# Kernel tuning notes

Hardware: AMD Instinct MI355X
Metric: run time of the kernel (lower is better)

The kernel has to match this reference:

```python
import jax, jax.numpy as jnp
import numpy as np

N_NODES = 100000


def gcn_conv(x, src, dst, W, b):
    # PyG GCNConv: add self-loops, symmetric deg^-1/2 normalization,
    # linear transform, scatter-add aggregation to target nodes, plus bias.
    n = x.shape[0]
    loops = jnp.arange(n, dtype=src.dtype)
    s = jnp.concatenate([src, loops])
    d = jnp.concatenate([dst, loops])
    deg = jax.ops.segment_sum(jnp.ones_like(s, dtype=x.dtype), d, num_segments=n)
    dinv = jnp.where(deg > 0, jax.lax.rsqrt(deg), 0.0)
    norm = dinv[s] * dinv[d]                       # [E+n]
    h = x @ W                                      # [n, out]
    msg = h[s] * norm[:, None]                     # gather + scale
    out = jax.ops.segment_sum(msg, d, num_segments=n)
    return out + b


def setup_inputs() -> dict:
    key = jax.random.key(0)
    k1, k2, k3, k4 = jax.random.split(key, 4)
    in_c, hid_c, out_c = 64, 64, 64
    n_edges = 1600000
    x = jax.random.normal(k1, (N_NODES, in_c), dtype=jnp.float32)
    edge_index = jax.random.randint(k2, (2, n_edges), 0, N_NODES, dtype=jnp.int64)
    W1 = jax.random.normal(k3, (in_c, hid_c), dtype=jnp.float32) * (1.0 / np.sqrt(in_c))
    b1 = jnp.zeros((hid_c,), dtype=jnp.float32)
    W2 = jax.random.normal(k4, (hid_c, out_c), dtype=jnp.float32) * (1.0 / np.sqrt(hid_c))
    b2 = jnp.zeros((out_c,), dtype=jnp.float32)
    return {"x": x, "edge_index": edge_index, "W1": W1, "b1": b1, "W2": W2, "b2": b2}


def reference(x, edge_index, W1, b1, W2, b2):
    src, dst = edge_index[0], edge_index[1]
    h = gcn_conv(x, src, dst, W1, b1)
    h = jax.nn.relu(h)
    out = gcn_conv(h, src, dst, W2, b2)
    return out
```

## Files before the change

### kernel.cpp

```cpp
#include <hip/hip_runtime.h>

#define NCH 64
#define NBLK 512
#define CB 512

typedef unsigned int uint;
typedef short short8 __attribute__((ext_vector_type(8)));
typedef float floatx4 __attribute__((ext_vector_type(4)));

__device__ inline uint bf16rne(float f) {
    uint u = __float_as_uint(f);
    return (u + 0x7fffu + ((u >> 16) & 1u)) >> 16;
}
__device__ inline uint pack2bf(float lo, float hi) {
    return bf16rne(lo) | (bf16rne(hi) << 16);
}
__device__ inline float unpLo(uint v) { return __uint_as_float(v << 16); }
__device__ inline float unpHi(uint v) { return __uint_as_float(v & 0xffff0000u); }


__global__ void coarse_hist_kernel(const int* __restrict__ dst, int* __restrict__ cntCB,
                                   int ne, int epb) {
    __shared__ int h[CB];
    int t = threadIdx.x;
    for (int i = t; i < CB; i += blockDim.x) h[i] = 0;
    __syncthreads();
    int e0 = blockIdx.x * epb;
    int e1 = min(e0 + epb, ne);
    for (int e = e0 + t; e < e1; e += blockDim.x)
        atomicAdd(&h[dst[e] >> 8], 1);
    __syncthreads();
    for (int i = t; i < CB; i += blockDim.x) cntCB[i * NBLK + blockIdx.x] = h[i];
}

__global__ void binscan_kernel(int* __restrict__ cntCB, int* __restrict__ binTot) {
    __shared__ int s[NBLK];
    int bin = blockIdx.x;
    int t = threadIdx.x;
    int v = cntCB[bin * NBLK + t];
    s[t] = v;
    __syncthreads();
    for (int off = 1; off < NBLK; off <<= 1) {
        int add = (t >= off) ? s[t - off] : 0;
        __syncthreads();
        s[t] += add;
        __syncthreads();
    }
    cntCB[bin * NBLK + t] = s[t] - v;
    if (t == NBLK - 1) binTot[bin] = s[t];
}

__global__ void cbscan_kernel(const int* __restrict__ binTot, int* __restrict__ cb,
                              int* __restrict__ rowptr, int n, int ne) {
    __shared__ int s[CB];
    int t = threadIdx.x;
    int v = binTot[t];
    s[t] = v;
    __syncthreads();
    for (int off = 1; off < CB; off <<= 1) {
        int add = (t >= off) ? s[t - off] : 0;
        __syncthreads();
        s[t] += add;
        __syncthreads();
    }
    cb[t] = s[t] - v;
    if (t == CB - 1) { cb[CB] = ne; rowptr[n] = ne; }
}

__global__ void coarse_scatter_kernel(const int* __restrict__ src, const int* __restrict__ dst,
                                      const int* __restrict__ cntCB, const int* __restrict__ cb,
                                      int2* __restrict__ coarse, int ne, int epb) {
    __shared__ int cur[CB];
    int t = threadIdx.x;
    for (int i = t; i < CB; i += blockDim.x)
        cur[i] = cb[i] + cntCB[i * NBLK + blockIdx.x];
    __syncthreads();
    int e0 = blockIdx.x * epb;
    int e1 = min(e0 + epb, ne);
    for (int e = e0 + t; e < e1; e += blockDim.x) {
        int d = dst[e];
        int pos = atomicAdd(&cur[d >> 8], 1);
        coarse[pos] = make_int2(d, src[e]);
    }
}

__global__ void bucket_kernel(const int2* __restrict__ coarse, const int* __restrict__ cb,
                              int* __restrict__ rowptr, float* __restrict__ dinv,
                              int* __restrict__ csr, int n) {
    __shared__ int hist[256];
    __shared__ int excl[256];
    __shared__ int cursor[256];
    int k = blockIdx.x;
    int t = threadIdx.x;
    int base = cb[k];
    int end = cb[k + 1];
    hist[t] = 0;
    __syncthreads();
    for (int i = base + t; i < end; i += 256)
        atomicAdd(&hist[coarse[i].x & 255], 1);
    __syncthreads();
    int v = hist[t];
    excl[t] = v;
    __syncthreads();
    for (int off = 1; off < 256; off <<= 1) {
        int add = (t >= off) ? excl[t - off] : 0;
        __syncthreads();
        excl[t] += add;
        __syncthreads();
    }
    int ex = excl[t] - v;
    int node = (k << 8) + t;
    if (node < n) {
        rowptr[node] = base + ex;
        dinv[node] = rsqrtf(1.0f + (float)v);
    }
    cursor[t] = base + ex;
    __syncthreads();
    for (int i = base + t; i < end; i += 256) {
        int2 e = coarse[i];
        int pos = atomicAdd(&cursor[e.x & 255], 1);
        csr[pos] = e.y;
    }
}

__global__ void wfrag_kernel(const float* __restrict__ W1, const float* __restrict__ W2,
                             uint4* __restrict__ frag) {
    int tid = blockIdx.x * blockDim.x + threadIdx.x;
    if (tid >= 1024) return;
    int mat = tid >> 9;
    int rem = tid & 511;
    int nt = rem >> 7;
    int kb = (rem >> 6) & 1;
    int lane = rem & 63;
    const float* W = mat ? W2 : W1;
    int kbase = kb * 32 + (lane >> 4) * 8;
    int col = nt * 16 + (lane & 15);
    uint r[4];
#pragma unroll
    for (int j = 0; j < 4; ++j) {
        float lo = W[(kbase + 2 * j) * NCH + col];
        float hi = W[(kbase + 2 * j + 1) * NCH + col];
        r[j] = pack2bf(lo, hi);
    }
    frag[tid] = make_uint4(r[0], r[1], r[2], r[3]);
}

template<bool RELU>
__global__ void gemm_mfma_kernel(const float* __restrict__ X, const uint4* __restrict__ wfrag,
                                 const float* __restrict__ dinv, uint* __restrict__ H, int n) {
    int lane = threadIdx.x & 63;
    int wave = blockIdx.x * (blockDim.x >> 6) + (threadIdx.x >> 6);
    int rb = wave * 16;
    if (rb >= n) return;

    short8 bfrag[4][2];
#pragma unroll
    for (int nt = 0; nt < 4; ++nt)
#pragma unroll
        for (int kb = 0; kb < 2; ++kb) {
            uint4 u = wfrag[(nt * 2 + kb) * 64 + lane];
            bfrag[nt][kb] = *(short8*)&u;
        }

    const float* xr = X + (long long)(rb + (lane & 15)) * NCH + (lane >> 4) * 8;
    short8 afrag[2];
#pragma unroll
    for (int kb = 0; kb < 2; ++kb) {
        float4 v0 = *(const float4*)(xr + kb * 32);
        float4 v1 = *(const float4*)(xr + kb * 32 + 4);
        if (RELU) {
            v0.x = fmaxf(v0.x, 0.f); v0.y = fmaxf(v0.y, 0.f);
            v0.z = fmaxf(v0.z, 0.f); v0.w = fmaxf(v0.w, 0.f);
            v1.x = fmaxf(v1.x, 0.f); v1.y = fmaxf(v1.y, 0.f);
            v1.z = fmaxf(v1.z, 0.f); v1.w = fmaxf(v1.w, 0.f);
        }
        short8 a;
        a[0] = (short)bf16rne(v0.x); a[1] = (short)bf16rne(v0.y);
        a[2] = (short)bf16rne(v0.z); a[3] = (short)bf16rne(v0.w);
        a[4] = (short)bf16rne(v1.x); a[5] = (short)bf16rne(v1.y);
        a[6] = (short)bf16rne(v1.z); a[7] = (short)bf16rne(v1.w);
        afrag[kb] = a;
    }

    floatx4 acc[4];
#pragma unroll
    for (int nt = 0; nt < 4; ++nt) acc[nt] = (floatx4){0.f, 0.f, 0.f, 0.f};
#pragma unroll
    for (int nt = 0; nt < 4; ++nt)
#pragma unroll
        for (int kb = 0; kb < 2; ++kb)
            acc[nt] = __builtin_amdgcn_mfma_f32_16x16x32_bf16(afrag[kb], bfrag[nt][kb], acc[nt], 0, 0, 0);

    int r0 = rb + (lane >> 4) * 4;
#pragma unroll
    for (int reg = 0; reg < 4; ++reg) {
        float di = dinv[r0 + reg];
        long long roww = (long long)(r0 + reg) * 32;
#pragma unroll
        for (int nt = 0; nt < 2; ++nt) {
            int w = nt * 16 + (lane & 15);
            H[roww + w] = pack2bf(di * acc[nt][reg], di * acc[nt + 2][reg]);
        }
    }
}

__global__ void agg_kernel(const uint* __restrict__ hsB, const int* __restrict__ rowptr,
                           const int* __restrict__ csr, const float* __restrict__ dinv,
                           const float* __restrict__ b, float* __restrict__ out, int n) {
    int wid = (blockIdx.x * blockDim.x + threadIdx.x) >> 6;
    if (wid >= n) return;
    wid = __builtin_amdgcn_readfirstlane(wid);
    int lane = threadIdx.x & 63;
    int q = lane >> 4;
    int u = lane & 15;
    int start = rowptr[wid];
    int end = rowptr[wid + 1];
    const uint2* __restrict__ base = (const uint2*)hsB + u;
    float ax0 = 0.f, ax1 = 0.f, ay0 = 0.f, ay1 = 0.f;
    if (q == 0) {
        uint2 v = base[(long long)wid * 16];
        ax0 = unpLo(v.x); ay0 = unpHi(v.x); ax1 = unpLo(v.y); ay1 = unpHi(v.y);
    }
    int eb = start;
    for (; eb + 16 <= end; eb += 16) {
        int s0 = csr[eb + q], s1 = csr[eb + q + 4], s2 = csr[eb + q + 8], s3 = csr[eb + q + 12];
        uint2 v0 = base[(long long)s0 * 16];
        uint2 v1 = base[(long long)s1 * 16];
        uint2 v2 = base[(long long)s2 * 16];
        uint2 v3 = base[(long long)s3 * 16];
        ax0 += (unpLo(v0.x) + unpLo(v1.x)) + (unpLo(v2.x) + unpLo(v3.x));
        ay0 += (unpHi(v0.x) + unpHi(v1.x)) + (unpHi(v2.x) + unpHi(v3.x));
        ax1 += (unpLo(v0.y) + unpLo(v1.y)) + (unpLo(v2.y) + unpLo(v3.y));
        ay1 += (unpHi(v0.y) + unpHi(v1.y)) + (unpHi(v2.y) + unpHi(v3.y));
    }
    if (eb < end) {
#pragma unroll
        for (int k = 0; k < 4; ++k) {
            int idx = eb + q + 4 * k;
            bool c = idx < end;
            int s = csr[idx];
            s = c ? s : 0;
            uint2 v = base[(long long)s * 16];
            ax0 += c ? unpLo(v.x) : 0.f;
            ay0 += c ? unpHi(v.x) : 0.f;
            ax1 += c ? unpLo(v.y) : 0.f;
            ay1 += c ? unpHi(v.y) : 0.f;
        }
    }
    ax0 += __shfl_xor(ax0, 16, 64); ay0 += __shfl_xor(ay0, 16, 64);
    ax1 += __shfl_xor(ax1, 16, 64); ay1 += __shfl_xor(ay1, 16, 64);
    ax0 += __shfl_xor(ax0, 32, 64); ay0 += __shfl_xor(ay0, 32, 64);
    ax1 += __shfl_xor(ax1, 32, 64); ay1 += __shfl_xor(ay1, 32, 64);
    if (q == 0) {
        float d = dinv[wid];
        float2 blo = *(const float2*)(b + 2 * u);
        float2 bhi = *(const float2*)(b + 2 * u + 32);
        *(float2*)(out + (long long)wid * NCH + 2 * u) =
            make_float2(d * ax0 + blo.x, d * ax1 + blo.y);
        *(float2*)(out + (long long)wid * NCH + 2 * u + 32) =
            make_float2(d * ay0 + bhi.x, d * ay1 + bhi.y);
    }
}

extern "C" void kernel_launch(void* const* d_in, const int* in_sizes, int n_in,
                              void* d_out, int out_size, void* d_ws, size_t ws_size,
                              hipStream_t stream) {
    const float* x  = (const float*)d_in[0];
    const int*   ei = (const int*)d_in[1];
    const float* W1 = (const float*)d_in[2];
    const float* b1 = (const float*)d_in[3];
    const float* W2 = (const float*)d_in[4];
    const float* b2 = (const float*)d_in[5];
    const int n  = in_sizes[0] / NCH;
    const int ne = in_sizes[1] / 2;
    const int* src = ei;
    const int* dst = ei + ne;
    float* out = (float*)d_out;

    char* ws = (char*)d_ws;
    size_t off = 0;
    auto alloc = [&](size_t bytes) { void* p = ws + off; off += (bytes + 255) & ~(size_t)255; return p; };
    int*   cntCB   = (int*)alloc((size_t)CB * NBLK * 4);
    int*   binTot  = (int*)alloc((size_t)CB * 4);
    int*   cb      = (int*)alloc((size_t)(CB + 1) * 4);
    int*   rowptr  = (int*)alloc((size_t)(n + 1) * 4);
    float* dinv    = (float*)alloc((size_t)n * 4);
    int*   csr     = (int*)alloc((size_t)ne * 4 + 64);
    int2*  coarse  = (int2*)alloc((size_t)ne * 8);
    uint*  hsB     = (uint*)alloc((size_t)n * 32 * 4);
    uint4* wfrag   = (uint4*)alloc(1024 * 16);

    const int blk = 256;
    const int gAgg = (n * 64 + blk - 1) / blk;
    const int epb  = (ne + NBLK - 1) / NBLK;
    const int nBuck = (n + 255) / 256;
    const int nWaveG = (n + 15) / 16;
    const int gGemm = (nWaveG + 3) / 4;

    wfrag_kernel         <<<4, 256, 0, stream>>>(W1, W2, wfrag);
    coarse_hist_kernel   <<<NBLK, blk, 0, stream>>>(dst, cntCB, ne, epb);
    binscan_kernel       <<<CB, NBLK, 0, stream>>>(cntCB, binTot);
    cbscan_kernel        <<<1, CB, 0, stream>>>(binTot, cb, rowptr, n, ne);
    coarse_scatter_kernel<<<NBLK, blk, 0, stream>>>(src, dst, cntCB, cb, coarse, ne, epb);
    bucket_kernel        <<<nBuck, 256, 0, stream>>>(coarse, cb, rowptr, dinv, csr, n);

    gemm_mfma_kernel<false><<<gGemm, blk, 0, stream>>>(x, wfrag, dinv, hsB, n);
    agg_kernel<<<gAgg, blk, 0, stream>>>(hsB, rowptr, csr, dinv, b1, out, n);

    gemm_mfma_kernel<true><<<gGemm, blk, 0, stream>>>(out, wfrag + 512, dinv, hsB, n);
    agg_kernel<<<gAgg, blk, 0, stream>>>(hsB, rowptr, csr, dinv, b2, out, n);
}
```

Before: 158.4 us.

## Store layer-1 activations as bf16 with fused ReLU and widen aggregation unroll

```diff
diff --git a/kernel.cpp b/kernel.cpp
--- a/kernel.cpp
+++ b/kernel.cpp
@@ -145,8 +145,8 @@
     frag[tid] = make_uint4(r[0], r[1], r[2], r[3]);
 }
 
-template<bool RELU>
-__global__ void gemm_mfma_kernel(const float* __restrict__ X, const uint4* __restrict__ wfrag,
+template<bool BF16A>
+__global__ void gemm_mfma_kernel(const void* __restrict__ Xv, const uint4* __restrict__ wfrag,
                                  const float* __restrict__ dinv, uint* __restrict__ H, int n) {
     int lane = threadIdx.x & 63;
     int wave = blockIdx.x * (blockDim.x >> 6) + (threadIdx.x >> 6);
@@ -162,24 +162,33 @@
             bfrag[nt][kb] = *(short8*)&u;
         }
 
-    const float* xr = X + (long long)(rb + (lane & 15)) * NCH + (lane >> 4) * 8;
     short8 afrag[2];
-#pragma unroll
-    for (int kb = 0; kb < 2; ++kb) {
-        float4 v0 = *(const float4*)(xr + kb * 32);
-        float4 v1 = *(const float4*)(xr + kb * 32 + 4);
-        if (RELU) {
-            v0.x = fmaxf(v0.x, 0.f); v0.y = fmaxf(v0.y, 0.f);
-            v0.z = fmaxf(v0.z, 0.f); v0.w = fmaxf(v0.w, 0.f);
-            v1.x = fmaxf(v1.x, 0.f); v1.y = fmaxf(v1.y, 0.f);
-            v1.z = fmaxf(v1.z, 0.f); v1.w = fmaxf(v1.w, 0.f);
-        }
-        short8 a;
-        a[0] = (short)bf16rne(v0.x); a[1] = (short)bf16rne(v0.y);
-        a[2] = (short)bf16rne(v0.z); a[3] = (short)bf16rne(v0.w);
-        a[4] = (short)bf16rne(v1.x); a[5] = (short)bf16rne(v1.y);
-        a[6] = (short)bf16rne(v1.z); a[7] = (short)bf16rne(v1.w);
-        afrag[kb] = a;
+    if (BF16A) {
+        const uint* hr = (const uint*)Xv + (long long)(rb + (lane & 15)) * 32 + (lane >> 4) * 8;
+        uint4 a0 = *(const uint4*)(hr);
+        uint4 a1 = *(const uint4*)(hr + 4);
+        uint w[8] = {a0.x, a0.y, a0.z, a0.w, a1.x, a1.y, a1.z, a1.w};
+        short8 f0, f1;
+#pragma unroll
+        for (int j = 0; j < 8; ++j) {
+            f0[j] = (short)(w[j] & 0xffffu);
+            f1[j] = (short)(w[j] >> 16);
+        }
+        afrag[0] = f0;
+        afrag[1] = f1;
+    } else {
+        const float* xr = (const float*)Xv + (long long)(rb + (lane & 15)) * NCH + (lane >> 4) * 8;
+#pragma unroll
+        for (int kb = 0; kb < 2; ++kb) {
+            float4 v0 = *(const float4*)(xr + kb * 32);
+            float4 v1 = *(const float4*)(xr + kb * 32 + 4);
+            short8 a;
+            a[0] = (short)bf16rne(v0.x); a[1] = (short)bf16rne(v0.y);
+            a[2] = (short)bf16rne(v0.z); a[3] = (short)bf16rne(v0.w);
+            a[4] = (short)bf16rne(v1.x); a[5] = (short)bf16rne(v1.y);
+            a[6] = (short)bf16rne(v1.z); a[7] = (short)bf16rne(v1.w);
+            afrag[kb] = a;
+        }
     }
 
     floatx4 acc[4];
@@ -204,9 +213,10 @@
     }
 }
 
+template<bool BF16OUT>
 __global__ void agg_kernel(const uint* __restrict__ hsB, const int* __restrict__ rowptr,
                            const int* __restrict__ csr, const float* __restrict__ dinv,
-                           const float* __restrict__ b, float* __restrict__ out, int n) {
+                           const float* __restrict__ b, void* __restrict__ outv, int n) {
     int wid = (blockIdx.x * blockDim.x + threadIdx.x) >> 6;
     if (wid >= n) return;
     wid = __builtin_amdgcn_readfirstlane(wid);
@@ -222,25 +232,38 @@
         ax0 = unpLo(v.x); ay0 = unpHi(v.x); ax1 = unpLo(v.y); ay1 = unpHi(v.y);
     }
     int eb = start;
-    for (; eb + 16 <= end; eb += 16) {
-        int s0 = csr[eb + q], s1 = csr[eb + q + 4], s2 = csr[eb + q + 8], s3 = csr[eb + q + 12];
-        uint2 v0 = base[(long long)s0 * 16];
-        uint2 v1 = base[(long long)s1 * 16];
-        uint2 v2 = base[(long long)s2 * 16];
-        uint2 v3 = base[(long long)s3 * 16];
-        ax0 += (unpLo(v0.x) + unpLo(v1.x)) + (unpLo(v2.x) + unpLo(v3.x));
-        ay0 += (unpHi(v0.x) + unpHi(v1.x)) + (unpHi(v2.x) + unpHi(v3.x));
-        ax1 += (unpLo(v0.y) + unpLo(v1.y)) + (unpLo(v2.y) + unpLo(v3.y));
-        ay1 += (unpHi(v0.y) + unpHi(v1.y)) + (unpHi(v2.y) + unpHi(v3.y));
+    for (; eb + 32 <= end; eb += 32) {
+        int4 i0, i1;
+        __builtin_memcpy(&i0, csr + eb + 4 * q, 16);
+        __builtin_memcpy(&i1, csr + eb + 16 + 4 * q, 16);
+        uint2 v0 = base[(long long)i0.x * 16];
+        uint2 v1 = base[(long long)i0.y * 16];
+        uint2 v2 = base[(long long)i0.z * 16];
+        uint2 v3 = base[(long long)i0.w * 16];
+        uint2 v4 = base[(long long)i1.x * 16];
+        uint2 v5 = base[(long long)i1.y * 16];
+        uint2 v6 = base[(long long)i1.z * 16];
+        uint2 v7 = base[(long long)i1.w * 16];
+        ax0 += ((unpLo(v0.x) + unpLo(v1.x)) + (unpLo(v2.x) + unpLo(v3.x)))
+             + ((unpLo(v4.x) + unpLo(v5.x)) + (unpLo(v6.x) + unpLo(v7.x)));
+        ay0 += ((unpHi(v0.x) + unpHi(v1.x)) + (unpHi(v2.x) + unpHi(v3.x)))
+             + ((unpHi(v4.x) + unpHi(v5.x)) + (unpHi(v6.x) + unpHi(v7.x)));
+        ax1 += ((unpLo(v0.y) + unpLo(v1.y)) + (unpLo(v2.y) + unpLo(v3.y)))
+             + ((unpLo(v4.y) + unpLo(v5.y)) + (unpLo(v6.y) + unpLo(v7.y)));
+        ay1 += ((unpHi(v0.y) + unpHi(v1.y)) + (unpHi(v2.y) + unpHi(v3.y)))
+             + ((unpHi(v4.y) + unpHi(v5.y)) + (unpHi(v6.y) + unpHi(v7.y)));
     }
     if (eb < end) {
-#pragma unroll
-        for (int k = 0; k < 4; ++k) {
-            int idx = eb + q + 4 * k;
+        int4 i0, i1;
+        __builtin_memcpy(&i0, csr + eb + 4 * q, 16);
+        __builtin_memcpy(&i1, csr + eb + 16 + 4 * q, 16);
+        int s[8] = {i0.x, i0.y, i0.z, i0.w, i1.x, i1.y, i1.z, i1.w};
+#pragma unroll
+        for (int k = 0; k < 8; ++k) {
+            int idx = eb + 16 * (k >> 2) + 4 * q + (k & 3);
             bool c = idx < end;
-            int s = csr[idx];
-            s = c ? s : 0;
-            uint2 v = base[(long long)s * 16];
+            int sk = c ? s[k] : 0;
+            uint2 v = base[(long long)sk * 16];
             ax0 += c ? unpLo(v.x) : 0.f;
             ay0 += c ? unpHi(v.x) : 0.f;
             ax1 += c ? unpLo(v.y) : 0.f;
@@ -255,10 +278,19 @@
         float d = dinv[wid];
         float2 blo = *(const float2*)(b + 2 * u);
         float2 bhi = *(const float2*)(b + 2 * u + 32);
-        *(float2*)(out + (long long)wid * NCH + 2 * u) =
-            make_float2(d * ax0 + blo.x, d * ax1 + blo.y);
-        *(float2*)(out + (long long)wid * NCH + 2 * u + 32) =
-            make_float2(d * ay0 + bhi.x, d * ay1 + bhi.y);
+        float r00 = d * ax0 + blo.x;
+        float r01 = d * ax1 + blo.y;
+        float r10 = d * ay0 + bhi.x;
+        float r11 = d * ay1 + bhi.y;
+        if (BF16OUT) {
+            uint w0 = pack2bf(fmaxf(r00, 0.f), fmaxf(r10, 0.f));
+            uint w1 = pack2bf(fmaxf(r01, 0.f), fmaxf(r11, 0.f));
+            *((uint2*)outv + (long long)wid * 16 + u) = make_uint2(w0, w1);
+        } else {
+            float* out = (float*)outv;
+            *(float2*)(out + (long long)wid * NCH + 2 * u) = make_float2(r00, r01);
+            *(float2*)(out + (long long)wid * NCH + 2 * u + 32) = make_float2(r10, r11);
+        }
     }
 }
 
@@ -275,7 +307,6 @@
     const int ne = in_sizes[1] / 2;
     const int* src = ei;
     const int* dst = ei + ne;
-    float* out = (float*)d_out;
 
     char* ws = (char*)d_ws;
     size_t off = 0;
@@ -285,9 +316,10 @@
     int*   cb      = (int*)alloc((size_t)(CB + 1) * 4);
     int*   rowptr  = (int*)alloc((size_t)(n + 1) * 4);
     float* dinv    = (float*)alloc((size_t)n * 4);
-    int*   csr     = (int*)alloc((size_t)ne * 4 + 64);
+    int*   csr     = (int*)alloc((size_t)ne * 4 + 128);
     int2*  coarse  = (int2*)alloc((size_t)ne * 8);
     uint*  hsB     = (uint*)alloc((size_t)n * 32 * 4);
+    uint*  hsB2    = (uint*)alloc((size_t)n * 32 * 4);
     uint4* wfrag   = (uint4*)alloc(1024 * 16);
 
     const int blk = 256;
@@ -305,8 +337,8 @@
     bucket_kernel        <<<nBuck, 256, 0, stream>>>(coarse, cb, rowptr, dinv, csr, n);
 
     gemm_mfma_kernel<false><<<gGemm, blk, 0, stream>>>(x, wfrag, dinv, hsB, n);
-    agg_kernel<<<gAgg, blk, 0, stream>>>(hsB, rowptr, csr, dinv, b1, out, n);
-
-    gemm_mfma_kernel<true><<<gGemm, blk, 0, stream>>>(out, wfrag + 512, dinv, hsB, n);
-    agg_kernel<<<gAgg, blk, 0, stream>>>(hsB, rowptr, csr, dinv, b2, out, n);
-}
+    agg_kernel<true><<<gAgg, blk, 0, stream>>>(hsB, rowptr, csr, dinv, b1, hsB2, n);
+
+    gemm_mfma_kernel<true><<<gGemm, blk, 0, stream>>>(hsB2, wfrag + 512, dinv, hsB, n);
+    agg_kernel<false><<<gAgg, blk, 0, stream>>>(hsB, rowptr, csr, dinv, b2, d_out, n);
+}
```

After: 158.2 us. Within noise of the previous version (-0.1%).
